# Kernel tuning notes

Hardware: AMD Instinct MI355X
Metric: run time of the kernel (lower is better)

Reference implementation:

```python
import jax, jax.numpy as jnp
import numpy as np

NUM_CLASS = 4096
HIDDEN = 512
N_GROUPS = 64  # per branch (co and cl)
BATCH = 64


def _make_group_of(rng, n_groups, num_class):
    # Ragged partition of [0, num_class) into n_groups contiguous segments,
    # mirroring len_co_list_index offsets of the original module.
    cuts = np.sort(rng.choice(np.arange(1, num_class), size=n_groups - 1, replace=False))
    sizes = np.diff(np.concatenate([[0], cuts, [num_class]]))
    return np.repeat(np.arange(n_groups), sizes)  # [num_class] -> group id per class slot


def setup_inputs() -> dict:
    key = jax.random.key(0)
    k_x, k_cow, k_clw, k_cob, k_clb = jax.random.split(key, 5)
    rng = np.random.default_rng(0)
    stdv = 1.0 / np.sqrt(HIDDEN)  # matches reset_parameters uniform(-stdv, stdv)

    x = jax.random.normal(k_x, (BATCH, 2 * N_GROUPS, HIDDEN), dtype=jnp.float32)
    co_W = jax.random.uniform(k_cow, (1, NUM_CLASS, HIDDEN), jnp.float32, -stdv, stdv)
    cl_W = jax.random.uniform(k_clw, (1, NUM_CLASS, HIDDEN), jnp.float32, -stdv, stdv)
    co_b = jax.random.uniform(k_cob, (1, NUM_CLASS), jnp.float32, -stdv, stdv)
    cl_b = jax.random.uniform(k_clb, (1, NUM_CLASS), jnp.float32, -stdv, stdv)

    co_group_of = jnp.asarray(_make_group_of(rng, N_GROUPS, NUM_CLASS), jnp.int32)
    cl_group_of = jnp.asarray(_make_group_of(rng, N_GROUPS, NUM_CLASS), jnp.int32)
    # co_index / cl_index are class-id permutations applied after concat
    co_index = jnp.asarray(rng.permutation(NUM_CLASS), jnp.int32)
    cl_index = jnp.asarray(rng.permutation(NUM_CLASS), jnp.int32)

    return {
        "x": x,
        "co_W": co_W, "cl_W": cl_W,
        "co_b": co_b, "cl_b": cl_b,
        "co_group_of": co_group_of, "cl_group_of": cl_group_of,
        "co_index": co_index, "cl_index": cl_index,
        "group_len": N_GROUPS,
    }


def reference(x, co_W, cl_W, co_b, cl_b, co_group_of, cl_group_of, co_index, cl_index, group_len):
    # x: [B, 2*G, H]; first G group-features feed the co branch, rest the cl branch.
    co_x = x[:, :group_len, :]   # [B, G, H]
    cl_x = x[:, group_len:, :]   # [B, G, H]

    # Fused ragged group-wise broadcast-multiply + reduce:
    # out[b, c] = dot(W[0, c], x[b, group_of[c]]) + b[0, c]
    co_out = jnp.einsum("bch,ch->bc", co_x[:, co_group_of, :], co_W[0]) + co_b  # [B, C]
    cl_out = jnp.einsum("bch,ch->bc", cl_x[:, cl_group_of, :], cl_W[0]) + cl_b  # [B, C]

    # Final index_select gather over classes
    return co_out[:, co_index], cl_out[:, cl_index]
```

## Files before the change

### kernel.cpp

```cpp
#include <hip/hip_runtime.h>
#include <hip/hip_bf16.h>
#include <string.h>

#define NUM_CLASS 4096
#define HIDDEN    512
#define NGROUPS   64
#define BATCH     64

#define WS_NWORK 0
#define WS_WORK  16
#define WS_SRC   2048
#define WS_INV   10240
#define TMP_OFF_F 32768
#define TMP_H_STRIDE (128*4096)
#define TMP_S_STRIDE (2*128*4096)

typedef __attribute__((ext_vector_type(8))) short short8;
typedef __attribute__((ext_vector_type(4))) float f32x4;

__device__ __forceinline__ unsigned int pack2bf(float a, float b) {
    __hip_bfloat16 ha = __float2bfloat16(a), hb = __float2bfloat16(b);
    unsigned short ua, ub;
    memcpy(&ua, &ha, 2); memcpy(&ub, &hb, 2);
    return (unsigned int)ua | ((unsigned int)ub << 16);
}

template<bool WITH_INV>
__global__ __launch_bounds__(1024) void prep_kernel(
    const int* __restrict__ co_gof, const int* __restrict__ cl_gof,
    const int* __restrict__ co_idx, const int* __restrict__ cl_idx,
    int* __restrict__ ws)
{
    __shared__ int s_starts[2][65];
    __shared__ int s_wbase[2][64];
    int tid = threadIdx.x;
    for (int v = tid; v < 2 * NUM_CLASS; v += 1024) {
        int h = v >> 12, c = v & (NUM_CLASS - 1);
        const int* gof = h ? cl_gof : co_gof;
        int g = gof[c];
        if (c == 0) { s_starts[h][0] = 0; s_starts[h][64] = NUM_CLASS; }
        else if (g != gof[c - 1]) s_starts[h][g] = c;
    }
    __syncthreads();
    if (tid < 64) {
        int lane = tid;
        for (int h = 0; h < 2; ++h) {
            int s = s_starts[h][lane], e = s_starts[h][lane + 1];
            int cnt = (e - s + 63) >> 6;
            int inc = cnt;
            #pragma unroll
            for (int d = 1; d < 64; d <<= 1) {
                int o = __shfl_up(inc, d, 64);
                if (lane >= d) inc += o;
            }
            int excl = inc - cnt;
            s_wbase[h][lane] = excl;
            for (int t = 0; t < cnt; ++t) {
                int c0 = s + t * 64;
                int ncls = min(64, e - c0);
                ws[WS_WORK + h * 128 + excl + t] = (lane << 20) | (ncls << 12) | c0;
            }
            if (lane == 63) ws[WS_NWORK + h] = inc;
        }
    }
    __syncthreads();
    for (int v = tid; v < 2 * NUM_CLASS; v += 1024) {
        int h = v >> 12, c = v & (NUM_CLASS - 1);
        const int* gof = h ? cl_gof : co_gof;
        int g = gof[c];
        int rel = c - s_starts[h][g];
        ws[WS_SRC + v] = (s_wbase[h][g] + (rel >> 6)) * 64 + (rel & 63);
        if (WITH_INV) {
            const int* idx = h ? cl_idx : co_idx;
            ws[WS_INV + h * NUM_CLASS + idx[c]] = c;
        }
    }
}

template<int KS, bool SCATTER>
__global__ __launch_bounds__(256, 4) void gwl_stage1(
    const float* __restrict__ x,
    const float* __restrict__ co_W, const float* __restrict__ cl_W,
    const float* __restrict__ co_b, const float* __restrict__ cl_b,
    int* __restrict__ ws, float* __restrict__ out)
{
    int widx = blockIdx.x, h = blockIdx.y, kh = blockIdx.z;
    int nw = ws[WS_NWORK + h];
    if (widx >= nw) return;
    int packed = ws[WS_WORK + h * 128 + widx];
    int c0 = packed & 0xFFF, ncls = (packed >> 12) & 0xFF, g = packed >> 20;
    const float* Wp = h ? cl_W : co_W;
    int xrow = h * 64 + g;

    __shared__ __align__(16) unsigned char smem[18432];
    unsigned short (*Xs)[72]  = (unsigned short(*)[72])smem;
    unsigned short (*Wls)[72] = (unsigned short(*)[72])(smem + 9216);

    int tid = threadIdx.x;
    int l = tid & 63, w = tid >> 6;

    int rowq[4], kvq[4], wcl[4];
    #pragma unroll
    for (int q = 0; q < 4; ++q) {
        int v = q * 256 + tid;
        rowq[q] = v >> 4;
        kvq[q]  = v & 15;
        wcl[q]  = min(rowq[q], ncls - 1);
    }

    float4 rx[4], rw[4];
    f32x4 acc[4];
    #pragma unroll
    for (int i = 0; i < 4; ++i) acc[i] = (f32x4)(0.0f);

    const int NCH = 8 / KS;
    const int kbase = kh * (HIDDEN / KS);

#define LOADC(K0) do {                                                              \
    int k0_ = (K0);                                                                 \
    _Pragma("unroll")                                                               \
    for (int q = 0; q < 4; ++q) {                                                   \
        rx[q] = *(const float4*)(x + rowq[q] * 65536 + xrow * 512 + k0_ + kvq[q]*4);\
        rw[q] = *(const float4*)(Wp + (c0 + wcl[q]) * 512 + k0_ + kvq[q] * 4);      \
    } } while (0)

#define STOREC() do {                                                               \
    _Pragma("unroll")                                                               \
    for (int q = 0; q < 4; ++q) {                                                   \
        unsigned int x0 = pack2bf(rx[q].x, rx[q].y);                                \
        unsigned int x1 = pack2bf(rx[q].z, rx[q].w);                                \
        unsigned int w0 = pack2bf(rw[q].x, rw[q].y);                                \
        unsigned int w1 = pack2bf(rw[q].z, rw[q].w);                                \
        *(uint2*)&Xs[rowq[q]][kvq[q] * 4]  = make_uint2(x0, x1);                    \
        *(uint2*)&Wls[rowq[q]][kvq[q] * 4] = make_uint2(w0, w1);                    \
    } } while (0)

#define COMPUTEC() do {                                                             \
    _Pragma("unroll")                                                               \
    for (int kq = 0; kq < 2; ++kq) {                                                \
        int koff = kq * 32 + (l >> 4) * 8;                                          \
        short8 bfrag = *(const short8*)&Wls[w * 16 + (l & 15)][koff];               \
        _Pragma("unroll")                                                           \
        for (int i = 0; i < 4; ++i) {                                               \
            short8 afrag = *(const short8*)&Xs[16 * i + (l & 15)][koff];            \
            acc[i] = __builtin_amdgcn_mfma_f32_16x16x32_bf16(afrag, bfrag, acc[i],  \
                                                             0, 0, 0);              \
        }                                                                           \
    } } while (0)

    LOADC(kbase);
    #pragma unroll 1
    for (int t = 0; t < NCH; ++t) {
        STOREC();
        __syncthreads();
        if (t + 1 < NCH) LOADC(kbase + (t + 1) * 64);
        COMPUTEC();
        __syncthreads();
    }

    float (*ftile)[65] = (float(*)[65])smem;
    #pragma unroll
    for (int i = 0; i < 4; ++i)
        #pragma unroll
        for (int r = 0; r < 4; ++r)
            ftile[w * 16 + (l & 15)][16 * i + (l >> 4) * 4 + r] = acc[i][r];
    __syncthreads();

    if (!SCATTER) {
        float* tile = (float*)ws + TMP_OFF_F
                    + (size_t)(kh * 2 + h) * TMP_H_STRIDE + (size_t)widx * 4096;
        #pragma unroll
        for (int p = 0; p < 4; ++p) {
            int f = p * 256 + tid;
            int slot = f >> 4, b4 = (f & 15) * 4;
            *(float4*)&tile[slot * 64 + b4] = *(const float4*)&ftile[slot][b4];
        }
    } else {
        const float* bias = h ? cl_b : co_b;
        const int*   inv  = ws + WS_INV + h * NUM_CLASS;
        float* outh = out + (size_t)h * BATCH * NUM_CLASS;
        #pragma unroll
        for (int p = 0; p < 4; ++p) {
            int f = p * 256 + tid;
            int slot = f >> 4, b4 = (f & 15) * 4;
            if (slot < ncls) {
                int c = c0 + slot;
                int oc = inv[c];
                float bb = bias[c];
                #pragma unroll
                for (int e = 0; e < 4; ++e)
                    outh[(b4 + e) * 4096 + oc] = ftile[slot][b4 + e] + bb;
            }
        }
    }
#undef LOADC
#undef STOREC
#undef COMPUTEC
}

template<int KS>
__global__ __launch_bounds__(256) void gwl_permute(
    const int* __restrict__ ws,
    const float* __restrict__ co_b, const float* __restrict__ cl_b,
    const int* __restrict__ co_idx, const int* __restrict__ cl_idx,
    float* __restrict__ out)
{
    int jc = blockIdx.x;
    int h  = blockIdx.y;
    const float* bias   = h ? cl_b : co_b;
    const int*   idx    = h ? cl_idx : co_idx;
    const int*   srcoff = ws + WS_SRC + h * NUM_CLASS;
    const float* tmph   = (const float*)ws + TMP_OFF_F + (size_t)h * TMP_H_STRIDE;

    __shared__ float tile[64][65];
    int tid = threadIdx.x;
    int lane = tid & 63, w = tid >> 6;

    #pragma unroll
    for (int u = 0; u < 16; ++u) {
        int jj = u * 4 + w;
        int j  = jc * 64 + jj;
        int c  = idx[j];
        int rc = srcoff[c];
        float v = bias[c];
        #pragma unroll
        for (int s = 0; s < KS; ++s)
            v += tmph[(size_t)s * TMP_S_STRIDE + (size_t)rc * 64 + lane];
        tile[lane][jj] = v;
    }
    __syncthreads();

    #pragma unroll
    for (int p = 0; p < 4; ++p) {
        int f = p * 256 + tid;
        int b = f >> 4, j4 = (f & 15) * 4;
        *(float4*)&out[((size_t)h * 64 + b) * 4096 + jc * 64 + j4] =
            *(const float4*)&tile[b][j4];
    }
}

extern "C" void kernel_launch(void* const* d_in, const int* in_sizes, int n_in,
                              void* d_out, int out_size, void* d_ws, size_t ws_size,
                              hipStream_t stream)
{
    (void)in_sizes; (void)n_in; (void)out_size;
    const float* x      = (const float*)d_in[0];
    const float* co_W   = (const float*)d_in[1];
    const float* cl_W   = (const float*)d_in[2];
    const float* co_b   = (const float*)d_in[3];
    const float* cl_b   = (const float*)d_in[4];
    const int*   co_gof = (const int*)d_in[5];
    const int*   cl_gof = (const int*)d_in[6];
    const int*   co_idx = (const int*)d_in[7];
    const int*   cl_idx = (const int*)d_in[8];
    int*   ws  = (int*)d_ws;
    float* out = (float*)d_out;

    const size_t base  = (size_t)TMP_OFF_F * 4;
    const size_t slice = (size_t)TMP_S_STRIDE * 4;

    if (ws_size >= base + 2 * slice) {
        hipLaunchKernelGGL((prep_kernel<false>), dim3(1), dim3(1024), 0, stream,
                           co_gof, cl_gof, co_idx, cl_idx, ws);
        hipLaunchKernelGGL((gwl_stage1<2, false>), dim3(128, 2, 2), dim3(256), 0, stream,
                           x, co_W, cl_W, co_b, cl_b, ws, out);
        hipLaunchKernelGGL((gwl_permute<2>), dim3(64, 2), dim3(256), 0, stream,
                           ws, co_b, cl_b, co_idx, cl_idx, out);
    } else if (ws_size >= base + 1 * slice) {
        hipLaunchKernelGGL((prep_kernel<false>), dim3(1), dim3(1024), 0, stream,
                           co_gof, cl_gof, co_idx, cl_idx, ws);
        hipLaunchKernelGGL((gwl_stage1<1, false>), dim3(128, 2, 1), dim3(256), 0, stream,
                           x, co_W, cl_W, co_b, cl_b, ws, out);
        hipLaunchKernelGGL((gwl_permute<1>), dim3(64, 2), dim3(256), 0, stream,
                           ws, co_b, cl_b, co_idx, cl_idx, out);
    } else {
        hipLaunchKernelGGL((prep_kernel<true>), dim3(1), dim3(1024), 0, stream,
                           co_gof, cl_gof, co_idx, cl_idx, ws);
        hipLaunchKernelGGL((gwl_stage1<1, true>), dim3(128, 2, 1), dim3(256), 0, stream,
                           x, co_W, cl_W, co_b, cl_b, ws, out);
    }
}
```

Baseline: 24.91 us.

## Double-buffer LDS tiles, prefetch two chunks ahead, and swizzle block order

The stage-1 kernel now keeps two LDS buffers and two register staging sets. Global loads for chunk t+2 and the LDS store for chunk t+1 are issued while chunk t is computed, which leaves one barrier per iteration instead of two. The grid is flattened to 1D, and block IDs are swizzled so consecutive blocks spread across the work/branch/k-split space, likely to spread them over XCDs. In exchange, LDS use doubles and register pressure rises, with launch bounds relaxed from 4 to 2 waves-per-SIMD-equivalent, so occupancy may fall.

```diff
diff --git a/kernel.cpp b/kernel.cpp
--- a/kernel.cpp
+++ b/kernel.cpp
@@ -78,13 +78,21 @@
 }
 
 template<int KS, bool SCATTER>
-__global__ __launch_bounds__(256, 4) void gwl_stage1(
+__global__ __launch_bounds__(256, 2) void gwl_stage1(
     const float* __restrict__ x,
     const float* __restrict__ co_W, const float* __restrict__ cl_W,
     const float* __restrict__ co_b, const float* __restrict__ cl_b,
     int* __restrict__ ws, float* __restrict__ out)
 {
-    int widx = blockIdx.x, h = blockIdx.y, kh = blockIdx.z;
+    const int nblk = 128 * 2 * KS;
+    const int chunk = nblk >> 3;
+    int bid = blockIdx.x;
+    int swz = (bid & 7) * chunk + (bid >> 3);
+    int widx = swz & 127;
+    int hk   = swz >> 7;
+    int h    = hk & 1;
+    int kh   = hk >> 1;
+
     int nw = ws[WS_NWORK + h];
     if (widx >= nw) return;
     int packed = ws[WS_WORK + h * 128 + widx];
@@ -92,9 +100,7 @@
     const float* Wp = h ? cl_W : co_W;
     int xrow = h * 64 + g;
 
-    __shared__ __align__(16) unsigned char smem[18432];
-    unsigned short (*Xs)[72]  = (unsigned short(*)[72])smem;
-    unsigned short (*Wls)[72] = (unsigned short(*)[72])(smem + 9216);
+    __shared__ __align__(16) unsigned char smem[2][18432];
 
     int tid = threadIdx.x;
     int l = tid & 63, w = tid >> 6;
@@ -108,7 +114,7 @@
         wcl[q]  = min(rowq[q], ncls - 1);
     }
 
-    float4 rx[4], rw[4];
+    float4 rxA[4], rwA[4], rxB[4], rwB[4];
     f32x4 acc[4];
     #pragma unroll
     for (int i = 0; i < 4; ++i) acc[i] = (f32x4)(0.0f);
@@ -116,49 +122,61 @@
     const int NCH = 8 / KS;
     const int kbase = kh * (HIDDEN / KS);
 
-#define LOADC(K0) do {                                                              \
-    int k0_ = (K0);                                                                 \
+#define LOADC(T, RX, RW) do {                                                       \
+    int k0_ = kbase + (T) * 64;                                                     \
     _Pragma("unroll")                                                               \
     for (int q = 0; q < 4; ++q) {                                                   \
-        rx[q] = *(const float4*)(x + rowq[q] * 65536 + xrow * 512 + k0_ + kvq[q]*4);\
-        rw[q] = *(const float4*)(Wp + (c0 + wcl[q]) * 512 + k0_ + kvq[q] * 4);      \
+        RX[q] = *(const float4*)(x + rowq[q] * 65536 + xrow * 512 + k0_ + kvq[q]*4);\
+        RW[q] = *(const float4*)(Wp + (c0 + wcl[q]) * 512 + k0_ + kvq[q] * 4);      \
     } } while (0)
 
-#define STOREC() do {                                                               \
+#define STOREC(BUF, RX, RW) do {                                                    \
+    unsigned short (*Xs_)[72]  = (unsigned short(*)[72])smem[BUF];                  \
+    unsigned short (*Wls_)[72] = (unsigned short(*)[72])(smem[BUF] + 9216);         \
     _Pragma("unroll")                                                               \
     for (int q = 0; q < 4; ++q) {                                                   \
-        unsigned int x0 = pack2bf(rx[q].x, rx[q].y);                                \
-        unsigned int x1 = pack2bf(rx[q].z, rx[q].w);                                \
-        unsigned int w0 = pack2bf(rw[q].x, rw[q].y);                                \
-        unsigned int w1 = pack2bf(rw[q].z, rw[q].w);                                \
-        *(uint2*)&Xs[rowq[q]][kvq[q] * 4]  = make_uint2(x0, x1);                    \
-        *(uint2*)&Wls[rowq[q]][kvq[q] * 4] = make_uint2(w0, w1);                    \
+        unsigned int x0 = pack2bf(RX[q].x, RX[q].y);                                \
+        unsigned int x1 = pack2bf(RX[q].z, RX[q].w);                                \
+        unsigned int w0 = pack2bf(RW[q].x, RW[q].y);                                \
+        unsigned int w1 = pack2bf(RW[q].z, RW[q].w);                                \
+        *(uint2*)&Xs_[rowq[q]][kvq[q] * 4]  = make_uint2(x0, x1);                   \
+        *(uint2*)&Wls_[rowq[q]][kvq[q] * 4] = make_uint2(w0, w1);                   \
     } } while (0)
 
-#define COMPUTEC() do {                                                             \
+#define COMPUTEC(BUF) do {                                                          \
+    unsigned short (*Xs_)[72]  = (unsigned short(*)[72])smem[BUF];                  \
+    unsigned short (*Wls_)[72] = (unsigned short(*)[72])(smem[BUF] + 9216);         \
     _Pragma("unroll")                                                               \
     for (int kq = 0; kq < 2; ++kq) {                                                \
         int koff = kq * 32 + (l >> 4) * 8;                                          \
-        short8 bfrag = *(const short8*)&Wls[w * 16 + (l & 15)][koff];               \
+        short8 bfrag = *(const short8*)&Wls_[w * 16 + (l & 15)][koff];              \
         _Pragma("unroll")                                                           \
         for (int i = 0; i < 4; ++i) {                                               \
-            short8 afrag = *(const short8*)&Xs[16 * i + (l & 15)][koff];            \
+            short8 afrag = *(const short8*)&Xs_[16 * i + (l & 15)][koff];           \
             acc[i] = __builtin_amdgcn_mfma_f32_16x16x32_bf16(afrag, bfrag, acc[i],  \
                                                              0, 0, 0);              \
         }                                                                           \
     } } while (0)
 
-    LOADC(kbase);
-    #pragma unroll 1
+    LOADC(0, rxA, rwA);
+    LOADC(1, rxB, rwB);
+    STOREC(0, rxA, rwA);
+    __syncthreads();
+    #pragma unroll
     for (int t = 0; t < NCH; ++t) {
-        STOREC();
+        if (t + 2 < NCH) {
+            if (t & 1) LOADC(t + 2, rxB, rwB);
+            else       LOADC(t + 2, rxA, rwA);
+        }
+        if (t + 1 < NCH) {
+            if (t & 1) STOREC((t + 1) & 1, rxA, rwA);
+            else       STOREC((t + 1) & 1, rxB, rwB);
+        }
+        COMPUTEC(t & 1);
         __syncthreads();
-        if (t + 1 < NCH) LOADC(kbase + (t + 1) * 64);
-        COMPUTEC();
-        __syncthreads();
-    }
-
-    float (*ftile)[65] = (float(*)[65])smem;
+    }
+
+    float (*ftile)[65] = (float(*)[65])smem[0];
     #pragma unroll
     for (int i = 0; i < 4; ++i)
         #pragma unroll
@@ -262,21 +280,21 @@
     if (ws_size >= base + 2 * slice) {
         hipLaunchKernelGGL((prep_kernel<false>), dim3(1), dim3(1024), 0, stream,
                            co_gof, cl_gof, co_idx, cl_idx, ws);
-        hipLaunchKernelGGL((gwl_stage1<2, false>), dim3(128, 2, 2), dim3(256), 0, stream,
+        hipLaunchKernelGGL((gwl_stage1<2, false>), dim3(512), dim3(256), 0, stream,
                            x, co_W, cl_W, co_b, cl_b, ws, out);
         hipLaunchKernelGGL((gwl_permute<2>), dim3(64, 2), dim3(256), 0, stream,
                            ws, co_b, cl_b, co_idx, cl_idx, out);
     } else if (ws_size >= base + 1 * slice) {
         hipLaunchKernelGGL((prep_kernel<false>), dim3(1), dim3(1024), 0, stream,
                            co_gof, cl_gof, co_idx, cl_idx, ws);
-        hipLaunchKernelGGL((gwl_stage1<1, false>), dim3(128, 2, 1), dim3(256), 0, stream,
+        hipLaunchKernelGGL((gwl_stage1<1, false>), dim3(256), dim3(256), 0, stream,
                            x, co_W, cl_W, co_b, cl_b, ws, out);
         hipLaunchKernelGGL((gwl_permute<1>), dim3(64, 2), dim3(256), 0, stream,
                            ws, co_b, cl_b, co_idx, cl_idx, out);
     } else {
         hipLaunchKernelGGL((prep_kernel<true>), dim3(1), dim3(1024), 0, stream,
                            co_gof, cl_gof, co_idx, cl_idx, ws);
-        hipLaunchKernelGGL((gwl_stage1<1, true>), dim3(128, 2, 1), dim3(256), 0, stream,
+        hipLaunchKernelGGL((gwl_stage1<1, true>), dim3(256), dim3(256), 0, stream,
                            x, co_W, cl_W, co_b, cl_b, ws, out);
     }
 }
```

After: 23.79 us. 1.05x faster.
